# Kernel optimization log

Hardware: AMD Instinct MI355X
Metric: run time of the kernel (lower is better)

The kernel has to match this reference:

```python
import jax, jax.numpy as jnp
import numpy as np
from jax import lax

N_EXPERTS = 256
N_GROUP = 8
TOPK_GROUP = 4
TOP_K = 8
AUX_ALPHA = 0.001


def setup_inputs() -> dict:
    key = jax.random.key(0)
    k1, k2 = jax.random.split(key)
    hidden_states = jax.random.normal(k1, (16384, 2048), dtype=jnp.float32)
    weight = jax.random.normal(k2, (N_EXPERTS, 2048), dtype=jnp.float32) * 0.02
    return {"hidden_states": hidden_states, "weight": weight}


def reference(hidden_states, weight):
    n_tokens = hidden_states.shape[0]
    group_size = N_EXPERTS // N_GROUP  # 32

    # gating logits: [N, E]
    logits = jnp.einsum('nh,eh->ne', hidden_states, weight)

    # group-restricted top-k: [N, G, group_size] -> top TOPK_GROUP per group
    group_logits = logits.reshape(n_tokens, N_GROUP, group_size)
    gw, gi = lax.top_k(group_logits, TOPK_GROUP)          # [N, G, tg]
    gw = gw.reshape(n_tokens, N_GROUP * TOPK_GROUP)
    gi = gi.reshape(n_tokens, N_GROUP * TOPK_GROUP)

    # global top-k over the pooled group winners
    topk_weights, ti = lax.top_k(gw, TOP_K)               # [N, K]
    selected_group = ti // TOPK_GROUP
    expert_in_group = jnp.take_along_axis(gi, ti, axis=1)
    topk_idx = selected_group * group_size + expert_in_group  # [N, K]

    # norm_topk_prob=True
    topk_weights = topk_weights / (jnp.sum(topk_weights, axis=-1, keepdims=True) + 1e-20)

    # auxiliary load-balancing loss (training path)
    expert_mask = jax.nn.one_hot(topk_idx.reshape(-1), N_EXPERTS, dtype=jnp.float32)
    expert_counts = expert_mask.mean(axis=0)              # [E]
    expert_probs = jax.nn.softmax(logits, axis=-1).mean(axis=0)  # [E]
    aux_loss = jnp.sum(expert_counts * expert_probs) * AUX_ALPHA

    return topk_idx, topk_weights, aux_loss
```

## Files before the change

### kernel.cpp

```cpp
#include <hip/hip_runtime.h>
#include <math.h>

#define NTOK 16384
#define KD   2048
#define NE   256
#define BM   64
#define NSTEP 64
#define EPS  2.5e-4f

using bf16x8 = __attribute__((ext_vector_type(8))) short;
using f32x16 = __attribute__((ext_vector_type(16))) float;
using u16 = unsigned short;
using u32 = unsigned int;

__device__ __forceinline__ u16 f2bf(float x) {
    u32 u = __float_as_uint(x);
    return (u16)((u + 0x7FFFu + ((u >> 16) & 1u)) >> 16);
}
__device__ __forceinline__ float bf2f(u16 h) {
    return __uint_as_float(((u32)h) << 16);
}

__global__ __launch_bounds__(256) void wsplit_kernel(
    const float* __restrict__ wgt, u16* __restrict__ Whi, u16* __restrict__ Wlo)
{
    const int idx = blockIdx.x * 256 + threadIdx.x;
    const int e = idx >> 11, k = idx & 2047;
    const int c = k >> 5, kk = k & 31;
    const float w = wgt[idx];
    const u16 hi = f2bf(w);
    const u16 lo = f2bf(w - bf2f(hi));
    const int off = c * 8192 + e * 32 + kk;
    Whi[off] = hi; Wlo[off] = lo;
}

__global__ __launch_bounds__(256) void gate_kernel(
    const float* __restrict__ hid, const u16* __restrict__ Whi, const u16* __restrict__ Wlo,
    float* __restrict__ out, float* __restrict__ cnt, float* __restrict__ prb,
    int* __restrict__ flagcnt, int* __restrict__ flaglist)
{
    __shared__ union {
        struct {
            u16 ah[2][64][40];
            u16 al[2][64][40];
            u16 bh[2][256][40];
            u16 bl[2][256][40];
        } st;
        float ls[64][257];
    } sh;
    __shared__ float maxS[64], sumS[64], invS[64];

    const int tid  = threadIdx.x;
    const int lane = tid & 63;
    const int wv   = tid >> 6;
    const int ln31 = lane & 31;
    const int kh8  = (lane >> 5) * 8;
    const int t0   = blockIdx.x * BM;

    f32x16 acc[2][2];
#pragma unroll
    for (int mf = 0; mf < 2; ++mf)
#pragma unroll
        for (int nf = 0; nf < 2; ++nf)
#pragma unroll
            for (int r = 0; r < 16; ++r) acc[mf][nf][r] = 0.f;

    float4 arg0, arg1;
    uint4 brgh[4], brgl[4];
    const int am  = tid >> 2;
    const int akq = (tid & 3) * 8;

    auto loadA = [&](int c) {
        const float* p = hid + (size_t)(t0 + am) * KD + c * 32 + akq;
        arg0 = *(const float4*)p;
        arg1 = *(const float4*)(p + 4);
    };
    auto loadB = [&](int c) {
        const u16* ph = Whi + c * 8192 + tid * 32;
        const u16* pl = Wlo + c * 8192 + tid * 32;
#pragma unroll
        for (int i = 0; i < 4; ++i) {
            brgh[i] = *(const uint4*)(ph + i * 8);
            brgl[i] = *(const uint4*)(pl + i * 8);
        }
    };
    auto writeA = [&](int buf) {
        float f[8] = {arg0.x, arg0.y, arg0.z, arg0.w, arg1.x, arg1.y, arg1.z, arg1.w};
        u16 hi[8], lo[8];
#pragma unroll
        for (int i = 0; i < 8; ++i) {
            hi[i] = f2bf(f[i]);
            lo[i] = f2bf(f[i] - bf2f(hi[i]));
        }
#pragma unroll
        for (int i = 0; i < 8; ++i) {
            sh.st.ah[buf][am][akq + i] = hi[i];
            sh.st.al[buf][am][akq + i] = lo[i];
        }
    };
    auto writeB = [&](int buf) {
#pragma unroll
        for (int i = 0; i < 4; ++i) {
            *(uint4*)&sh.st.bh[buf][tid][i * 8] = brgh[i];
            *(uint4*)&sh.st.bl[buf][tid][i * 8] = brgl[i];
        }
    };

    loadA(0); loadB(0);
    writeA(0); writeB(0);
    int cur = 0;

#pragma unroll 1
    for (int c = 0; c < NSTEP; ++c) {
        __syncthreads();
        const int nxt = cur ^ 1;
        if (c + 1 < NSTEP) { loadA(c + 1); loadB(c + 1); }

#pragma unroll
        for (int s = 0; s < 2; ++s) {
            bf16x8 ah[2], al2[2], bh[2], bl2[2];
#pragma unroll
            for (int mf = 0; mf < 2; ++mf) {
                const int r = mf * 32 + ln31;
                ah[mf]  = *(const bf16x8*)&sh.st.ah[cur][r][s * 16 + kh8];
                al2[mf] = *(const bf16x8*)&sh.st.al[cur][r][s * 16 + kh8];
            }
#pragma unroll
            for (int nf = 0; nf < 2; ++nf) {
                const int r = wv * 64 + nf * 32 + ln31;
                bh[nf]  = *(const bf16x8*)&sh.st.bh[cur][r][s * 16 + kh8];
                bl2[nf] = *(const bf16x8*)&sh.st.bl[cur][r][s * 16 + kh8];
            }
#pragma unroll
            for (int mf = 0; mf < 2; ++mf)
#pragma unroll
                for (int nf = 0; nf < 2; ++nf) {
                    acc[mf][nf] = __builtin_amdgcn_mfma_f32_32x32x16_bf16(ah[mf],  bh[nf],  acc[mf][nf], 0, 0, 0);
                    acc[mf][nf] = __builtin_amdgcn_mfma_f32_32x32x16_bf16(ah[mf],  bl2[nf], acc[mf][nf], 0, 0, 0);
                    acc[mf][nf] = __builtin_amdgcn_mfma_f32_32x32x16_bf16(al2[mf], bh[nf],  acc[mf][nf], 0, 0, 0);
                }
        }
        if (c + 1 < NSTEP) { writeA(nxt); writeB(nxt); }
        cur = nxt;
    }

    __syncthreads();
#pragma unroll
    for (int mf = 0; mf < 2; ++mf)
#pragma unroll
        for (int nf = 0; nf < 2; ++nf) {
            const int col = wv * 64 + nf * 32 + ln31;
#pragma unroll
            for (int r = 0; r < 16; ++r) {
                const int row = mf * 32 + (r & 3) + 8 * (r >> 2) + 4 * (lane >> 5);
                sh.ls[row][col] = acc[mf][nf][r];
            }
        }
    if (tid < 64) sumS[tid] = 0.f;
    __syncthreads();

    if (tid < 64) {
        const float* lr = &sh.ls[tid][0];
        float tv[9]; int ti[9];
#pragma unroll
        for (int j = 0; j < 9; ++j) { tv[j] = -1e30f; ti[j] = 0; }
        float gv3[8], gv4[8];
        float rowmax = -1e30f;

        auto ins9 = [&](float v, int idx) {
#pragma unroll
            for (int p = 0; p < 9; ++p) {
                if (v > tv[p]) {
#pragma unroll
                    for (int q = 8; q > p; --q) { tv[q] = tv[q - 1]; ti[q] = ti[q - 1]; }
                    tv[p] = v; ti[p] = idx;
                    break;
                }
            }
        };

#pragma unroll 1
        for (int g = 0; g < 8; ++g) {
            float v0 = -1e30f, v1 = -1e30f, v2 = -1e30f, v3 = -1e30f, v4 = -1e30f;
            int   i0 = 0, i1 = 0, i2 = 0, i3 = 0;
            for (int j = 0; j < 32; ++j) {
                const float v = lr[g * 32 + j];
                if (v > v0)      { v4=v3; v3=v2;i3=i2; v2=v1;i2=i1; v1=v0;i1=i0; v0=v;i0=j; }
                else if (v > v1) { v4=v3; v3=v2;i3=i2; v2=v1;i2=i1; v1=v;i1=j; }
                else if (v > v2) { v4=v3; v3=v2;i3=i2; v2=v;i2=j; }
                else if (v > v3) { v4=v3; v3=v;i3=j; }
                else if (v > v4) { v4=v; }
            }
            rowmax = fmaxf(rowmax, v0);
            gv3[g] = v3; gv4[g] = v4;
            ins9(v0, g * 32 + i0);
            ins9(v1, g * 32 + i1);
            ins9(v2, g * 32 + i2);
            ins9(v3, g * 32 + i3);
        }

        bool flag = false;
#pragma unroll
        for (int r = 0; r < 8; ++r)
            if (tv[r] - tv[r + 1] < EPS) flag = true;
#pragma unroll
        for (int g = 0; g < 8; ++g)
            if (gv3[g] - gv4[g] < EPS && gv3[g] > tv[7] - EPS) flag = true;

        const float s01 = __fadd_rn(tv[0], tv[1]);
        const float s23 = __fadd_rn(tv[2], tv[3]);
        const float s45 = __fadd_rn(tv[4], tv[5]);
        const float s67 = __fadd_rn(tv[6], tv[7]);
        float s = __fadd_rn(__fadd_rn(s01, s23), __fadd_rn(s45, s67));
        s = __fadd_rn(s, 1e-20f);

        const size_t tg2 = (size_t)(t0 + tid);
#pragma unroll
        for (int j = 0; j < 8; ++j) {
            out[tg2 * 8 + j]                    = (float)ti[j];
            out[(size_t)NTOK * 8 + tg2 * 8 + j] = __fdiv_rn(tv[j], s);
            atomicAdd(&cnt[ti[j]], 1.0f);
        }
        if (flag) {
            const int fi = atomicAdd(flagcnt, 1);
            flaglist[fi] = t0 + tid;
        }
        maxS[tid] = rowmax;
    }
    __syncthreads();

    {
        const int t  = tid & 63;
        const int c0 = (tid >> 6) * 64;
        const float m = maxS[t];
        float part = 0.f;
#pragma unroll
        for (int j = 0; j < 64; ++j) part += __expf(sh.ls[t][c0 + j] - m);
        atomicAdd(&sumS[t], part);
    }
    __syncthreads();
    if (tid < 64) invS[tid] = 1.0f / sumS[tid];
    __syncthreads();

    {
        float p = 0.f;
#pragma unroll
        for (int n = 0; n < 64; ++n) p += __expf(sh.ls[n][tid] - maxS[n]) * invS[n];
        atomicAdd(&prb[tid], p);
    }
}

__global__ __launch_bounds__(256) void exact_kernel(
    const float* __restrict__ hid, const float* __restrict__ wgt,
    float* __restrict__ out, float* __restrict__ cnt,
    const int* __restrict__ flagcnt, const int* __restrict__ flaglist)
{
    const int fn = *flagcnt;
    const int base = blockIdx.x * 8;
    if (base >= fn) return;
    const int nt = min(8, fn - base);

    __shared__ float wch[256 * 17];
    __shared__ float hch[8 * 17];
    __shared__ float exls[8][257];
    __shared__ int tk[8];

    const int tid = threadIdx.x;
    const int tg  = tid >> 7;
    const int eg  = (tid >> 2) & 31;
    const int l   = tid & 3;

    if (tid < 8) tk[tid] = (tid < nt) ? flaglist[base + tid] : flaglist[base];
    __syncthreads();

    float accq[4][8];
#pragma unroll
    for (int i = 0; i < 4; ++i)
#pragma unroll
        for (int j = 0; j < 8; ++j) accq[i][j] = 0.f;

#pragma unroll 1
    for (int c = 0; c < 128; ++c) {
        __syncthreads();
        {
            const float* p = wgt + (size_t)tid * KD + c * 16;
            float4 w0 = *(const float4*)(p);
            float4 w1 = *(const float4*)(p + 4);
            float4 w2 = *(const float4*)(p + 8);
            float4 w3 = *(const float4*)(p + 12);
            float* wr = &wch[tid * 17];
            wr[0]=w0.x; wr[1]=w0.y; wr[2]=w0.z; wr[3]=w0.w;
            wr[4]=w1.x; wr[5]=w1.y; wr[6]=w1.z; wr[7]=w1.w;
            wr[8]=w2.x; wr[9]=w2.y; wr[10]=w2.z; wr[11]=w2.w;
            wr[12]=w3.x; wr[13]=w3.y; wr[14]=w3.z; wr[15]=w3.w;
        }
        if (tid < 128) {
            const int tok = tid >> 4, k = tid & 15;
            hch[tok * 17 + k] = hid[(size_t)tk[tok] * KD + c * 16 + k];
        }
        __syncthreads();

#pragma unroll
        for (int q = 3; q >= 0; --q) {
            const int k = 4 * q + l;
            float hv[4], wv2[8];
#pragma unroll
            for (int i = 0; i < 4; ++i) hv[i] = hch[(tg * 4 + i) * 17 + k];
#pragma unroll
            for (int j = 0; j < 8; ++j) wv2[j] = wch[(j * 32 + eg) * 17 + k];
#pragma unroll
            for (int i = 0; i < 4; ++i)
#pragma unroll
                for (int j = 0; j < 8; ++j)
                    accq[i][j] = __fadd_rn(__fmul_rn(hv[i], wv2[j]), accq[i][j]);
        }
    }

    __syncthreads();
#pragma unroll
    for (int i = 0; i < 4; ++i)
#pragma unroll
        for (int j = 0; j < 8; ++j) {
            float v = accq[i][j];
            v = __fadd_rn(v, __shfl_xor(v, 1));
            v = __fadd_rn(v, __shfl_xor(v, 2));
            if (l == 0) exls[tg * 4 + i][j * 32 + eg] = v;
        }
    __syncthreads();

    if (tid < nt) {
        const float* lr = &exls[tid][0];
        float tv[8]; int ti[8];
#pragma unroll
        for (int j = 0; j < 8; ++j) { tv[j] = -1e30f; ti[j] = 0; }

        auto ins8 = [&](float v, int idx) {
#pragma unroll
            for (int p = 0; p < 8; ++p) {
                if (v > tv[p]) {
#pragma unroll
                    for (int q = 7; q > p; --q) { tv[q] = tv[q - 1]; ti[q] = ti[q - 1]; }
                    tv[p] = v; ti[p] = idx;
                    break;
                }
            }
        };

#pragma unroll 1
        for (int g = 0; g < 8; ++g) {
            float v0 = -1e30f, v1 = -1e30f, v2 = -1e30f, v3 = -1e30f;
            int   i0 = 0, i1 = 0, i2 = 0, i3 = 0;
            for (int j = 0; j < 32; ++j) {
                const float v = lr[g * 32 + j];
                if (v > v0)      { v3=v2;i3=i2; v2=v1;i2=i1; v1=v0;i1=i0; v0=v;i0=j; }
                else if (v > v1) { v3=v2;i3=i2; v2=v1;i2=i1; v1=v;i1=j; }
                else if (v > v2) { v3=v2;i3=i2; v2=v;i2=j; }
                else if (v > v3) { v3=v;i3=j; }
            }
            ins8(v0, g * 32 + i0);
            ins8(v1, g * 32 + i1);
            ins8(v2, g * 32 + i2);
            ins8(v3, g * 32 + i3);
        }

        const float s01 = __fadd_rn(tv[0], tv[1]);
        const float s23 = __fadd_rn(tv[2], tv[3]);
        const float s45 = __fadd_rn(tv[4], tv[5]);
        const float s67 = __fadd_rn(tv[6], tv[7]);
        float s = __fadd_rn(__fadd_rn(s01, s23), __fadd_rn(s45, s67));
        s = __fadd_rn(s, 1e-20f);

        const size_t gt = (size_t)tk[tid];
#pragma unroll
        for (int j = 0; j < 8; ++j) {
            const int oldi = (int)out[gt * 8 + j];
            if (oldi != ti[j]) {
                atomicAdd(&cnt[oldi], -1.0f);
                atomicAdd(&cnt[ti[j]], 1.0f);
            }
            out[gt * 8 + j]                    = (float)ti[j];
            out[(size_t)NTOK * 8 + gt * 8 + j] = __fdiv_rn(tv[j], s);
        }
    }
}

__global__ void aux_kernel(const float* __restrict__ cnt,
                           const float* __restrict__ prb,
                           float* __restrict__ out)
{
    const int tid = threadIdx.x;
    float v = cnt[tid] * prb[tid];
#pragma unroll
    for (int off = 32; off; off >>= 1) v += __shfl_down(v, off, 64);
    __shared__ float ps[4];
    if ((tid & 63) == 0) ps[tid >> 6] = v;
    __syncthreads();
    if (tid == 0) {
        const float tot = ps[0] + ps[1] + ps[2] + ps[3];
        out[(size_t)NTOK * 8 * 2] = tot * (0.001f / (131072.0f * 16384.0f));
    }
}

extern "C" void kernel_launch(void* const* d_in, const int* in_sizes, int n_in,
                              void* d_out, int out_size, void* d_ws, size_t ws_size,
                              hipStream_t stream)
{
    (void)in_sizes; (void)n_in; (void)out_size; (void)ws_size;
    const float* hid = (const float*)d_in[0];
    const float* wgt = (const float*)d_in[1];
    float* out = (float*)d_out;

    float* cnt      = (float*)d_ws;
    float* prb      = cnt + NE;
    int*   flagcnt  = (int*)(prb + NE);
    int*   flaglist = flagcnt + 64;
    u16*   Whi      = (u16*)(flaglist + NTOK);
    u16*   Wlo      = Whi + (size_t)NE * KD;

    hipMemsetAsync(d_ws, 0, (2 * NE + 64) * sizeof(float), stream);
    wsplit_kernel<<<2048, 256, 0, stream>>>(wgt, Whi, Wlo);
    gate_kernel<<<NTOK / BM, 256, 0, stream>>>(hid, Whi, Wlo, out, cnt, prb, flagcnt, flaglist);
    exact_kernel<<<NTOK / 8, 256, 0, stream>>>(hid, wgt, out, cnt, flagcnt, flaglist);
    aux_kernel<<<1, 256, 0, stream>>>(cnt, prb, out);
}
```

Measured before the change: 554.1 us.

## Stream weight fragments directly from global memory and shrink gate tile to 32 tokens

The weight split kernel now writes the bf16 hi/lo weights in an MFMA-fragment-ready layout. The gate kernel then loads B operands straight from global/L2 into registers instead of staging them through LDS, and halves the token tile to 32 with a 4-blocks-per-CU launch bound. This removes the large B staging buffers and their LDS traffic, raising occupancy. The cost is twice as many blocks re-reading the weights from cache. The exact-recompute kernel becomes a persistent grid of 64 blocks that loops over flagged tokens instead of launching one block per possible group.

```diff
diff --git a/kernel.cpp b/kernel.cpp
--- a/kernel.cpp
+++ b/kernel.cpp
@@ -4,7 +4,7 @@
 #define NTOK 16384
 #define KD   2048
 #define NE   256
-#define BM   64
+#define BM   32
 #define NSTEP 64
 #define EPS  2.5e-4f
 
@@ -25,30 +25,34 @@
     const float* __restrict__ wgt, u16* __restrict__ Whi, u16* __restrict__ Wlo)
 {
     const int idx = blockIdx.x * 256 + threadIdx.x;
-    const int e = idx >> 11, k = idx & 2047;
-    const int c = k >> 5, kk = k & 31;
-    const float w = wgt[idx];
-    const u16 hi = f2bf(w);
-    const u16 lo = f2bf(w - bf2f(hi));
-    const int off = c * 8192 + e * 32 + kk;
-    Whi[off] = hi; Wlo[off] = lo;
-}
-
-__global__ __launch_bounds__(256) void gate_kernel(
+    const int e  = idx >> 8;
+    const int ko = idx & 255;
+    const int k  = ko * 8;
+    const int c  = k >> 5, s = (k >> 4) & 1, kh = (k >> 3) & 1;
+    const int dst = (c * 2 + s) * 4096 + (e >> 6) * 1024 + ((e >> 5) & 1) * 512
+                  + kh * 256 + (e & 31) * 8;
+    const float* p = wgt + (size_t)e * KD + k;
+    u16 hi[8], lo[8];
+#pragma unroll
+    for (int i = 0; i < 8; ++i) {
+        const float w = p[i];
+        hi[i] = f2bf(w);
+        lo[i] = f2bf(w - bf2f(hi[i]));
+    }
+    *(uint4*)(Whi + dst) = *(const uint4*)hi;
+    *(uint4*)(Wlo + dst) = *(const uint4*)lo;
+}
+
+__global__ __launch_bounds__(256, 4) void gate_kernel(
     const float* __restrict__ hid, const u16* __restrict__ Whi, const u16* __restrict__ Wlo,
     float* __restrict__ out, float* __restrict__ cnt, float* __restrict__ prb,
     int* __restrict__ flagcnt, int* __restrict__ flaglist)
 {
     __shared__ union {
-        struct {
-            u16 ah[2][64][40];
-            u16 al[2][64][40];
-            u16 bh[2][256][40];
-            u16 bl[2][256][40];
-        } st;
-        float ls[64][257];
+        struct { u16 ah[2][BM][40]; u16 al[2][BM][40]; } st;
+        float ls[BM][257];
     } sh;
-    __shared__ float maxS[64], sumS[64], invS[64];
+    __shared__ float maxS[BM], sumS[BM], invS[BM];
 
     const int tid  = threadIdx.x;
     const int lane = tid & 63;
@@ -57,109 +61,75 @@
     const int kh8  = (lane >> 5) * 8;
     const int t0   = blockIdx.x * BM;
 
-    f32x16 acc[2][2];
-#pragma unroll
-    for (int mf = 0; mf < 2; ++mf)
-#pragma unroll
-        for (int nf = 0; nf < 2; ++nf)
-#pragma unroll
-            for (int r = 0; r < 16; ++r) acc[mf][nf][r] = 0.f;
-
-    float4 arg0, arg1;
-    uint4 brgh[4], brgl[4];
-    const int am  = tid >> 2;
-    const int akq = (tid & 3) * 8;
+    f32x16 acc[2];
+#pragma unroll
+    for (int nf = 0; nf < 2; ++nf)
+#pragma unroll
+        for (int r = 0; r < 16; ++r) acc[nf][r] = 0.f;
+
+    float4 areg;
+    const int am = tid >> 3;
+    const int ak = (tid & 7) * 4;
 
     auto loadA = [&](int c) {
-        const float* p = hid + (size_t)(t0 + am) * KD + c * 32 + akq;
-        arg0 = *(const float4*)p;
-        arg1 = *(const float4*)(p + 4);
-    };
-    auto loadB = [&](int c) {
-        const u16* ph = Whi + c * 8192 + tid * 32;
-        const u16* pl = Wlo + c * 8192 + tid * 32;
-#pragma unroll
-        for (int i = 0; i < 4; ++i) {
-            brgh[i] = *(const uint4*)(ph + i * 8);
-            brgl[i] = *(const uint4*)(pl + i * 8);
-        }
+        areg = *(const float4*)(hid + (size_t)(t0 + am) * KD + c * 32 + ak);
     };
     auto writeA = [&](int buf) {
-        float f[8] = {arg0.x, arg0.y, arg0.z, arg0.w, arg1.x, arg1.y, arg1.z, arg1.w};
-        u16 hi[8], lo[8];
-#pragma unroll
-        for (int i = 0; i < 8; ++i) {
-            hi[i] = f2bf(f[i]);
-            lo[i] = f2bf(f[i] - bf2f(hi[i]));
-        }
-#pragma unroll
-        for (int i = 0; i < 8; ++i) {
-            sh.st.ah[buf][am][akq + i] = hi[i];
-            sh.st.al[buf][am][akq + i] = lo[i];
+        float f[4] = {areg.x, areg.y, areg.z, areg.w};
+#pragma unroll
+        for (int i = 0; i < 4; ++i) {
+            const u16 hi = f2bf(f[i]);
+            sh.st.ah[buf][am][ak + i] = hi;
+            sh.st.al[buf][am][ak + i] = f2bf(f[i] - bf2f(hi));
         }
     };
-    auto writeB = [&](int buf) {
-#pragma unroll
-        for (int i = 0; i < 4; ++i) {
-            *(uint4*)&sh.st.bh[buf][tid][i * 8] = brgh[i];
-            *(uint4*)&sh.st.bl[buf][tid][i * 8] = brgl[i];
-        }
-    };
-
-    loadA(0); loadB(0);
-    writeA(0); writeB(0);
+
+    loadA(0); writeA(0);
     int cur = 0;
 
 #pragma unroll 1
     for (int c = 0; c < NSTEP; ++c) {
         __syncthreads();
         const int nxt = cur ^ 1;
-        if (c + 1 < NSTEP) { loadA(c + 1); loadB(c + 1); }
-
+        if (c + 1 < NSTEP) loadA(c + 1);
+
+        const u16* bbase = (const u16*)0;
 #pragma unroll
         for (int s = 0; s < 2; ++s) {
-            bf16x8 ah[2], al2[2], bh[2], bl2[2];
-#pragma unroll
-            for (int mf = 0; mf < 2; ++mf) {
-                const int r = mf * 32 + ln31;
-                ah[mf]  = *(const bf16x8*)&sh.st.ah[cur][r][s * 16 + kh8];
-                al2[mf] = *(const bf16x8*)&sh.st.al[cur][r][s * 16 + kh8];
-            }
-#pragma unroll
-            for (int nf = 0; nf < 2; ++nf) {
-                const int r = wv * 64 + nf * 32 + ln31;
-                bh[nf]  = *(const bf16x8*)&sh.st.bh[cur][r][s * 16 + kh8];
-                bl2[nf] = *(const bf16x8*)&sh.st.bl[cur][r][s * 16 + kh8];
-            }
-#pragma unroll
-            for (int mf = 0; mf < 2; ++mf)
-#pragma unroll
-                for (int nf = 0; nf < 2; ++nf) {
-                    acc[mf][nf] = __builtin_amdgcn_mfma_f32_32x32x16_bf16(ah[mf],  bh[nf],  acc[mf][nf], 0, 0, 0);
-                    acc[mf][nf] = __builtin_amdgcn_mfma_f32_32x32x16_bf16(ah[mf],  bl2[nf], acc[mf][nf], 0, 0, 0);
-                    acc[mf][nf] = __builtin_amdgcn_mfma_f32_32x32x16_bf16(al2[mf], bh[nf],  acc[mf][nf], 0, 0, 0);
-                }
-        }
-        if (c + 1 < NSTEP) { writeA(nxt); writeB(nxt); }
+            const int boff = (c * 2 + s) * 4096 + wv * 1024 + lane * 8;
+            const bf16x8 bh0 = *(const bf16x8*)(Whi + boff);
+            const bf16x8 bl0 = *(const bf16x8*)(Wlo + boff);
+            const bf16x8 bh1 = *(const bf16x8*)(Whi + boff + 512);
+            const bf16x8 bl1 = *(const bf16x8*)(Wlo + boff + 512);
+            const bf16x8 ah  = *(const bf16x8*)&sh.st.ah[cur][ln31][s * 16 + kh8];
+            const bf16x8 al  = *(const bf16x8*)&sh.st.al[cur][ln31][s * 16 + kh8];
+
+            acc[0] = __builtin_amdgcn_mfma_f32_32x32x16_bf16(ah, bh0, acc[0], 0, 0, 0);
+            acc[0] = __builtin_amdgcn_mfma_f32_32x32x16_bf16(ah, bl0, acc[0], 0, 0, 0);
+            acc[0] = __builtin_amdgcn_mfma_f32_32x32x16_bf16(al, bh0, acc[0], 0, 0, 0);
+            acc[1] = __builtin_amdgcn_mfma_f32_32x32x16_bf16(ah, bh1, acc[1], 0, 0, 0);
+            acc[1] = __builtin_amdgcn_mfma_f32_32x32x16_bf16(ah, bl1, acc[1], 0, 0, 0);
+            acc[1] = __builtin_amdgcn_mfma_f32_32x32x16_bf16(al, bh1, acc[1], 0, 0, 0);
+        }
+        (void)bbase;
+        if (c + 1 < NSTEP) writeA(nxt);
         cur = nxt;
     }
 
     __syncthreads();
 #pragma unroll
-    for (int mf = 0; mf < 2; ++mf)
-#pragma unroll
-        for (int nf = 0; nf < 2; ++nf) {
-            const int col = wv * 64 + nf * 32 + ln31;
-#pragma unroll
-            for (int r = 0; r < 16; ++r) {
-                const int row = mf * 32 + (r & 3) + 8 * (r >> 2) + 4 * (lane >> 5);
-                sh.ls[row][col] = acc[mf][nf][r];
-            }
-        }
-    if (tid < 64) sumS[tid] = 0.f;
-    __syncthreads();
-
-    if (tid < 64) {
+    for (int nf = 0; nf < 2; ++nf) {
+        const int col = wv * 64 + nf * 32 + ln31;
+#pragma unroll
+        for (int r = 0; r < 16; ++r) {
+            const int row = (r & 3) + 8 * (r >> 2) + 4 * (lane >> 5);
+            sh.ls[row][col] = acc[nf][r];
+        }
+    }
+    if (tid < BM) sumS[tid] = 0.f;
+    __syncthreads();
+
+    if (tid < BM) {
         const float* lr = &sh.ls[tid][0];
         float tv[9]; int ti[9];
 #pragma unroll
@@ -230,22 +200,22 @@
     __syncthreads();
 
     {
-        const int t  = tid & 63;
-        const int c0 = (tid >> 6) * 64;
+        const int t  = tid >> 3;
+        const int c0 = (tid & 7) * 32;
         const float m = maxS[t];
         float part = 0.f;
 #pragma unroll
-        for (int j = 0; j < 64; ++j) part += __expf(sh.ls[t][c0 + j] - m);
+        for (int j = 0; j < 32; ++j) part += __expf(sh.ls[t][c0 + j] - m);
         atomicAdd(&sumS[t], part);
     }
     __syncthreads();
-    if (tid < 64) invS[tid] = 1.0f / sumS[tid];
+    if (tid < BM) invS[tid] = 1.0f / sumS[tid];
     __syncthreads();
 
     {
         float p = 0.f;
 #pragma unroll
-        for (int n = 0; n < 64; ++n) p += __expf(sh.ls[n][tid] - maxS[n]) * invS[n];
+        for (int n = 0; n < BM; ++n) p += __expf(sh.ls[n][tid] - maxS[n]) * invS[n];
         atomicAdd(&prb[tid], p);
     }
 }
@@ -256,9 +226,6 @@
     const int* __restrict__ flagcnt, const int* __restrict__ flaglist)
 {
     const int fn = *flagcnt;
-    const int base = blockIdx.x * 8;
-    if (base >= fn) return;
-    const int nt = min(8, fn - base);
 
     __shared__ float wch[256 * 17];
     __shared__ float hch[8 * 17];
@@ -270,117 +237,123 @@
     const int eg  = (tid >> 2) & 31;
     const int l   = tid & 3;
 
-    if (tid < 8) tk[tid] = (tid < nt) ? flaglist[base + tid] : flaglist[base];
-    __syncthreads();
-
-    float accq[4][8];
-#pragma unroll
-    for (int i = 0; i < 4; ++i)
-#pragma unroll
-        for (int j = 0; j < 8; ++j) accq[i][j] = 0.f;
-
-#pragma unroll 1
-    for (int c = 0; c < 128; ++c) {
-        __syncthreads();
-        {
-            const float* p = wgt + (size_t)tid * KD + c * 16;
-            float4 w0 = *(const float4*)(p);
-            float4 w1 = *(const float4*)(p + 4);
-            float4 w2 = *(const float4*)(p + 8);
-            float4 w3 = *(const float4*)(p + 12);
-            float* wr = &wch[tid * 17];
-            wr[0]=w0.x; wr[1]=w0.y; wr[2]=w0.z; wr[3]=w0.w;
-            wr[4]=w1.x; wr[5]=w1.y; wr[6]=w1.z; wr[7]=w1.w;
-            wr[8]=w2.x; wr[9]=w2.y; wr[10]=w2.z; wr[11]=w2.w;
-            wr[12]=w3.x; wr[13]=w3.y; wr[14]=w3.z; wr[15]=w3.w;
-        }
-        if (tid < 128) {
-            const int tok = tid >> 4, k = tid & 15;
-            hch[tok * 17 + k] = hid[(size_t)tk[tok] * KD + c * 16 + k];
-        }
-        __syncthreads();
-
-#pragma unroll
-        for (int q = 3; q >= 0; --q) {
-            const int k = 4 * q + l;
-            float hv[4], wv2[8];
-#pragma unroll
-            for (int i = 0; i < 4; ++i) hv[i] = hch[(tg * 4 + i) * 17 + k];
-#pragma unroll
-            for (int j = 0; j < 8; ++j) wv2[j] = wch[(j * 32 + eg) * 17 + k];
-#pragma unroll
-            for (int i = 0; i < 4; ++i)
-#pragma unroll
-                for (int j = 0; j < 8; ++j)
-                    accq[i][j] = __fadd_rn(__fmul_rn(hv[i], wv2[j]), accq[i][j]);
-        }
-    }
-
-    __syncthreads();
-#pragma unroll
-    for (int i = 0; i < 4; ++i)
-#pragma unroll
-        for (int j = 0; j < 8; ++j) {
-            float v = accq[i][j];
-            v = __fadd_rn(v, __shfl_xor(v, 1));
-            v = __fadd_rn(v, __shfl_xor(v, 2));
-            if (l == 0) exls[tg * 4 + i][j * 32 + eg] = v;
-        }
-    __syncthreads();
-
-    if (tid < nt) {
-        const float* lr = &exls[tid][0];
-        float tv[8]; int ti[8];
-#pragma unroll
-        for (int j = 0; j < 8; ++j) { tv[j] = -1e30f; ti[j] = 0; }
-
-        auto ins8 = [&](float v, int idx) {
-#pragma unroll
-            for (int p = 0; p < 8; ++p) {
-                if (v > tv[p]) {
-#pragma unroll
-                    for (int q = 7; q > p; --q) { tv[q] = tv[q - 1]; ti[q] = ti[q - 1]; }
-                    tv[p] = v; ti[p] = idx;
-                    break;
+#pragma unroll 1
+    for (int base = blockIdx.x * 8; base < fn; base += 64 * 8) {
+        const int nt = min(8, fn - base);
+        __syncthreads();
+        if (tid < 8) tk[tid] = (tid < nt) ? flaglist[base + tid] : flaglist[base];
+        __syncthreads();
+
+        float accq[4][8];
+#pragma unroll
+        for (int i = 0; i < 4; ++i)
+#pragma unroll
+            for (int j = 0; j < 8; ++j) accq[i][j] = 0.f;
+
+#pragma unroll 1
+        for (int c = 0; c < 128; ++c) {
+            __syncthreads();
+            {
+                const float* p = wgt + (size_t)tid * KD + c * 16;
+                float4 w0 = *(const float4*)(p);
+                float4 w1 = *(const float4*)(p + 4);
+                float4 w2 = *(const float4*)(p + 8);
+                float4 w3 = *(const float4*)(p + 12);
+                float* wr = &wch[tid * 17];
+                wr[0]=w0.x; wr[1]=w0.y; wr[2]=w0.z; wr[3]=w0.w;
+                wr[4]=w1.x; wr[5]=w1.y; wr[6]=w1.z; wr[7]=w1.w;
+                wr[8]=w2.x; wr[9]=w2.y; wr[10]=w2.z; wr[11]=w2.w;
+                wr[12]=w3.x; wr[13]=w3.y; wr[14]=w3.z; wr[15]=w3.w;
+            }
+            if (tid < 128) {
+                const int tok = tid >> 4, k = tid & 15;
+                hch[tok * 17 + k] = hid[(size_t)tk[tok] * KD + c * 16 + k];
+            }
+            __syncthreads();
+
+#pragma unroll
+            for (int q = 3; q >= 0; --q) {
+                const int k = 4 * q + l;
+                float hv[4], wv2[8];
+#pragma unroll
+                for (int i = 0; i < 4; ++i) hv[i] = hch[(tg * 4 + i) * 17 + k];
+#pragma unroll
+                for (int j = 0; j < 8; ++j) wv2[j] = wch[(j * 32 + eg) * 17 + k];
+#pragma unroll
+                for (int i = 0; i < 4; ++i)
+#pragma unroll
+                    for (int j = 0; j < 8; ++j)
+                        accq[i][j] = __fadd_rn(__fmul_rn(hv[i], wv2[j]), accq[i][j]);
+            }
+        }
+
+        __syncthreads();
+#pragma unroll
+        for (int i = 0; i < 4; ++i)
+#pragma unroll
+            for (int j = 0; j < 8; ++j) {
+                float v = accq[i][j];
+                v = __fadd_rn(v, __shfl_xor(v, 1));
+                v = __fadd_rn(v, __shfl_xor(v, 2));
+                if (l == 0) exls[tg * 4 + i][j * 32 + eg] = v;
+            }
+        __syncthreads();
+
+        if (tid < nt) {
+            const float* lr = &exls[tid][0];
+            float tv[8]; int ti[8];
+#pragma unroll
+            for (int j = 0; j < 8; ++j) { tv[j] = -1e30f; ti[j] = 0; }
+
+            auto ins8 = [&](float v, int idx) {
+#pragma unroll
+                for (int p = 0; p < 8; ++p) {
+                    if (v > tv[p]) {
+#pragma unroll
+                        for (int q = 7; q > p; --q) { tv[q] = tv[q - 1]; ti[q] = ti[q - 1]; }
+                        tv[p] = v; ti[p] = idx;
+                        break;
+                    }
                 }
-            }
-        };
-
-#pragma unroll 1
-        for (int g = 0; g < 8; ++g) {
-            float v0 = -1e30f, v1 = -1e30f, v2 = -1e30f, v3 = -1e30f;
-            int   i0 = 0, i1 = 0, i2 = 0, i3 = 0;
-            for (int j = 0; j < 32; ++j) {
-                const float v = lr[g * 32 + j];
-                if (v > v0)      { v3=v2;i3=i2; v2=v1;i2=i1; v1=v0;i1=i0; v0=v;i0=j; }
-                else if (v > v1) { v3=v2;i3=i2; v2=v1;i2=i1; v1=v;i1=j; }
-                else if (v > v2) { v3=v2;i3=i2; v2=v;i2=j; }
-                else if (v > v3) { v3=v;i3=j; }
-            }
-            ins8(v0, g * 32 + i0);
-            ins8(v1, g * 32 + i1);
-            ins8(v2, g * 32 + i2);
-            ins8(v3, g * 32 + i3);
-        }
-
-        const float s01 = __fadd_rn(tv[0], tv[1]);
-        const float s23 = __fadd_rn(tv[2], tv[3]);
-        const float s45 = __fadd_rn(tv[4], tv[5]);
-        const float s67 = __fadd_rn(tv[6], tv[7]);
-        float s = __fadd_rn(__fadd_rn(s01, s23), __fadd_rn(s45, s67));
-        s = __fadd_rn(s, 1e-20f);
-
-        const size_t gt = (size_t)tk[tid];
-#pragma unroll
-        for (int j = 0; j < 8; ++j) {
-            const int oldi = (int)out[gt * 8 + j];
-            if (oldi != ti[j]) {
-                atomicAdd(&cnt[oldi], -1.0f);
-                atomicAdd(&cnt[ti[j]], 1.0f);
-            }
-            out[gt * 8 + j]                    = (float)ti[j];
-            out[(size_t)NTOK * 8 + gt * 8 + j] = __fdiv_rn(tv[j], s);
-        }
+            };
+
+#pragma unroll 1
+            for (int g = 0; g < 8; ++g) {
+                float v0 = -1e30f, v1 = -1e30f, v2 = -1e30f, v3 = -1e30f;
+                int   i0 = 0, i1 = 0, i2 = 0, i3 = 0;
+                for (int j = 0; j < 32; ++j) {
+                    const float v = lr[g * 32 + j];
+                    if (v > v0)      { v3=v2;i3=i2; v2=v1;i2=i1; v1=v0;i1=i0; v0=v;i0=j; }
+                    else if (v > v1) { v3=v2;i3=i2; v2=v1;i2=i1; v1=v;i1=j; }
+                    else if (v > v2) { v3=v2;i3=i2; v2=v;i2=j; }
+                    else if (v > v3) { v3=v;i3=j; }
+                }
+                ins8(v0, g * 32 + i0);
+                ins8(v1, g * 32 + i1);
+                ins8(v2, g * 32 + i2);
+                ins8(v3, g * 32 + i3);
+            }
+
+            const float s01 = __fadd_rn(tv[0], tv[1]);
+            const float s23 = __fadd_rn(tv[2], tv[3]);
+            const float s45 = __fadd_rn(tv[4], tv[5]);
+            const float s67 = __fadd_rn(tv[6], tv[7]);
+            float s = __fadd_rn(__fadd_rn(s01, s23), __fadd_rn(s45, s67));
+            s = __fadd_rn(s, 1e-20f);
+
+            const size_t gt = (size_t)tk[tid];
+#pragma unroll
+            for (int j = 0; j < 8; ++j) {
+                const int oldi = (int)out[gt * 8 + j];
+                if (oldi != ti[j]) {
+                    atomicAdd(&cnt[oldi], -1.0f);
+                    atomicAdd(&cnt[ti[j]], 1.0f);
+                }
+                out[gt * 8 + j]                    = (float)ti[j];
+                out[(size_t)NTOK * 8 + gt * 8 + j] = __fdiv_rn(tv[j], s);
+            }
+        }
+        __syncthreads();
     }
 }
 
@@ -418,8 +391,8 @@
     u16*   Wlo      = Whi + (size_t)NE * KD;
 
     hipMemsetAsync(d_ws, 0, (2 * NE + 64) * sizeof(float), stream);
-    wsplit_kernel<<<2048, 256, 0, stream>>>(wgt, Whi, Wlo);
+    wsplit_kernel<<<NE * KD / 8 / 256, 256, 0, stream>>>(wgt, Whi, Wlo);
     gate_kernel<<<NTOK / BM, 256, 0, stream>>>(hid, Whi, Wlo, out, cnt, prb, flagcnt, flaglist);
-    exact_kernel<<<NTOK / 8, 256, 0, stream>>>(hid, wgt, out, cnt, flagcnt, flaglist);
+    exact_kernel<<<64, 256, 0, stream>>>(hid, wgt, out, cnt, flagcnt, flaglist);
     aux_kernel<<<1, 256, 0, stream>>>(cnt, prb, out);
 }
```

After: 493.2 us. -11.0%, faster.
